# Kernel tuning notes

Measured on AMD Instinct MI355X. Metric: run time of the kernel, lower is better.

Reference implementation:

```python
import jax, jax.numpy as jnp
import numpy as np

EPS = 1e-5
DIM = 128
SCALE = DIM ** (-0.5)


def setup_inputs() -> dict:
    key = jax.random.key(0)
    k1, k2, k3 = jax.random.split(key, 3)
    B, N, D = 2, 128 * 128, DIM
    Q = N // 4
    x = jax.random.normal(k1, (B, N, D), dtype=jnp.float32)
    gamma = jnp.ones((D,), dtype=jnp.float32)
    beta = jnp.zeros((D,), dtype=jnp.float32)
    queries = jax.random.normal(k2, (Q, D), dtype=jnp.float32)
    W = jax.random.normal(k3, (2 * D, D), dtype=jnp.float32) * (1.0 / np.sqrt(D))
    return {"x": x, "gamma": gamma, "beta": beta, "queries": queries, "W": W}


def reference(x, gamma, beta, queries, W):
    # LayerNorm over last dim (eps matches torch default 1e-5)
    mu = jnp.mean(x, axis=-1, keepdims=True)
    var = jnp.mean(jnp.square(x - mu), axis=-1, keepdims=True)
    xn = (x - mu) * jax.lax.rsqrt(var + EPS) * gamma + beta  # [B, N, D]
    # learned-query cross attention: sim = Q @ xn^T * scale -> softmax -> @ xn
    sim = jnp.einsum('qd,bnd->bqn', queries, xn) * SCALE     # [B, Q, N]
    attn = jax.nn.softmax(sim, axis=-1)
    out = jnp.einsum('bqn,bnd->bqd', attn, xn)               # [B, Q, D]
    # trailing linear: dim -> 2*dim, no bias
    return jnp.einsum('bqd,ed->bqe', out, W)                 # [B, Q, 2D]
```

## Files before the change

### kernel.cpp

```cpp
#include <hip/hip_runtime.h>
#include <stdint.h>

#define Nn 16384
#define Dd 128
#define Qq 4096
#define Ee 256
#define NSPLIT 8
#define NCHUNK 2048
#define KV 64
#define NITER 32

typedef __bf16 bf16x8 __attribute__((ext_vector_type(8)));
typedef float floatx16 __attribute__((ext_vector_type(16)));

__device__ __forceinline__ float fexp2(float x) {
#if __has_builtin(__builtin_amdgcn_exp2f)
  return __builtin_amdgcn_exp2f(x);
#else
  return exp2f(x);
#endif
}
__device__ __forceinline__ unsigned pk_bf(float lo, float hi) {
  return __builtin_amdgcn_perm(__float_as_uint(hi) + 0x8000u,
                               __float_as_uint(lo) + 0x8000u, 0x07060302u);
}
__device__ __forceinline__ void stage16(const void* g, void* lds_uniform) {
  __builtin_amdgcn_global_load_lds(
      (const __attribute__((address_space(1))) unsigned int*)g,
      (__attribute__((address_space(3))) unsigned int*)lds_uniform, 16, 0, 0);
}

__global__ __launch_bounds__(256) void k_lnt(
    const float* __restrict__ x, const float* __restrict__ gamma,
    const float* __restrict__ beta, const float* __restrict__ queries,
    const float* __restrict__ W, unsigned* __restrict__ xn,
    unsigned short* __restrict__ xnT, unsigned short* __restrict__ qb,
    unsigned short* __restrict__ wb) {
  __shared__ __align__(16) uint2 lds2[64 * 32];
  const int tid = threadIdx.x;
  const int bid = blockIdx.x;
  const int b = bid >> 8, n0 = (bid & 255) * 64;
  const int r = tid >> 2, qd = tid & 3;

  const float4* xp = (const float4*)(x + ((size_t)(b * Nn + n0 + r)) * Dd + qd * 32);
  float4 v[8];
  float s = 0.f, s2 = 0.f;
#pragma unroll
  for (int i = 0; i < 8; ++i) {
    v[i] = xp[i];
    s += (v[i].x + v[i].y) + (v[i].z + v[i].w);
    s2 += (v[i].x * v[i].x + v[i].y * v[i].y) + (v[i].z * v[i].z + v[i].w * v[i].w);
  }
  s += __shfl_xor(s, 1); s2 += __shfl_xor(s2, 1);
  s += __shfl_xor(s, 2); s2 += __shfl_xor(s2, 2);
  float mu = s * (1.0f / 128.0f);
  float var = s2 * (1.0f / 128.0f) - mu * mu;
  float rs = rsqrtf(var + 1e-5f);

  const float4* gp = (const float4*)(gamma + qd * 32);
  const float4* bp = (const float4*)(beta + qd * 32);
  unsigned pk[16];
#pragma unroll
  for (int i = 0; i < 8; ++i) {
    float4 g = gp[i], bt = bp[i];
    pk[2 * i] = pk_bf((v[i].x - mu) * rs * g.x + bt.x, (v[i].y - mu) * rs * g.y + bt.y);
    pk[2 * i + 1] = pk_bf((v[i].z - mu) * rs * g.z + bt.z, (v[i].w - mu) * rs * g.w + bt.w);
  }
  unsigned* xrow = xn + ((size_t)(b * Nn + n0 + r)) * 64;
#pragma unroll
  for (int j = 0; j < 4; ++j)
    *(uint4*)(xrow + (((qd * 4 + j) ^ (r & 7)) * 4)) =
        make_uint4(pk[4 * j], pk[4 * j + 1], pk[4 * j + 2], pk[4 * j + 3]);
  const int rk = r & 31;
#pragma unroll
  for (int kk = 0; kk < 8; ++kk)
    lds2[r * 32 + ((qd * 8 + kk) ^ rk)] = make_uint2(pk[2 * kk], pk[2 * kk + 1]);
  __syncthreads();
  const int dq = tid >> 3, nc = tid & 7;
  uint2 U[8];
#pragma unroll
  for (int j = 0; j < 8; ++j) {
    int rr = nc * 8 + j;
    U[j] = lds2[rr * 32 + (dq ^ (rr & 31))];
  }
#pragma unroll
  for (int e = 0; e < 4; ++e) {
    int d = dq * 4 + e;
    unsigned a0 = (e & 2) ? U[0].y : U[0].x, a1 = (e & 2) ? U[1].y : U[1].x;
    unsigned a2 = (e & 2) ? U[2].y : U[2].x, a3 = (e & 2) ? U[3].y : U[3].x;
    unsigned a4 = (e & 2) ? U[4].y : U[4].x, a5 = (e & 2) ? U[5].y : U[5].x;
    unsigned a6 = (e & 2) ? U[6].y : U[6].x, a7 = (e & 2) ? U[7].y : U[7].x;
    unsigned sel = (e & 1) ? 0x07060302u : 0x05040100u;
    uint4 o;
    o.x = __builtin_amdgcn_perm(a1, a0, sel);
    o.y = __builtin_amdgcn_perm(a3, a2, sel);
    o.z = __builtin_amdgcn_perm(a5, a4, sel);
    o.w = __builtin_amdgcn_perm(a7, a6, sel);
    *(uint4*)(xnT + ((size_t)(b * Dd + d)) * Nn + n0 + (nc ^ (d & 7)) * 8) = o;
  }
  const float QSC = 0.08838834764831845f * 1.4426950408889634f;
  const int total4 = (Qq * Dd + Ee * Dd) / 4;
  for (int u = bid * 256 + tid; u < total4; u += 512 * 256) {
    if (u < Qq * Dd / 4) {
      float4 v4 = ((const float4*)queries)[u];
      ((uint2*)qb)[u] = make_uint2(pk_bf(v4.x * QSC, v4.y * QSC),
                                   pk_bf(v4.z * QSC, v4.w * QSC));
    } else {
      float4 v4 = ((const float4*)W)[u - Qq * Dd / 4];
      ((uint2*)wb)[u - Qq * Dd / 4] =
          make_uint2(pk_bf(v4.x, v4.y), pk_bf(v4.z, v4.w));
    }
  }
}

__global__ __launch_bounds__(256, 2) void k_attn(
    const unsigned short* __restrict__ xn,
    const unsigned short* __restrict__ xnT,
    const unsigned short* __restrict__ qb,
    float* __restrict__ o_part,
    float* __restrict__ l_part) {
  __shared__ __align__(16) char lds[49152];
  char* lds_x = lds;
  char* lds_xt = lds + 16384;
  char* lds_p = lds + 32768;

  const int bid = blockIdx.x;
  const int split = bid & 7, qt = (bid >> 3) & 31, b = bid >> 8;
  const int tid = threadIdx.x;
  const int wave = tid >> 6, lane = tid & 63;
  const int col = lane & 31, half = lane >> 5;
  const int ck = col & 7;
  const int qwbase = qt * 128 + wave * 32;

  bf16x8 qf[8];
#pragma unroll
  for (int s = 0; s < 8; ++s)
    qf[s] = *(const bf16x8*)(qb + (size_t)(qwbase + col) * Dd + s * 16 + half * 8);

  const floatx16 fz = {0.f,0.f,0.f,0.f,0.f,0.f,0.f,0.f,0.f,0.f,0.f,0.f,0.f,0.f,0.f,0.f};
  floatx16 O[4];
#pragma unroll
  for (int d = 0; d < 4; ++d) O[d] = fz;
  float lsum = 0.f;

  const char* gx = (const char*)xn + (size_t)b * Nn * 256;
  const char* gxt = (const char*)xnT + (size_t)b * Dd * Nn * 2;
  char* ldsp_w = lds_p + wave * 4096;

  for (int i = 0; i < NITER; ++i) {
    const int nb = split * NCHUNK + i * KV;
    const char* xsrc = gx + (size_t)nb * 256;
#pragma unroll
    for (int p = 0; p < 4; ++p) {
      int m = wave * 4 + p;
      stage16(xsrc + m * 1024 + lane * 16, lds_x + m * 1024);
    }
#pragma unroll
    for (int p = 0; p < 4; ++p) {
      int m = wave * 4 + p;
      const char* g = gxt + (size_t)(m * 8 + (lane >> 3)) * (Nn * 2) +
                      (size_t)nb * 2 + (lane & 7) * 16;
      stage16(g, lds_xt + m * 1024);
    }
    __syncthreads();

    floatx16 S[2];
    S[0] = fz; S[1] = fz;
#pragma unroll
    for (int s = 0; s < 8; ++s)
#pragma unroll
      for (int mt = 0; mt < 2; ++mt) {
        bf16x8 ax = *(const bf16x8*)(lds_x + (32 * mt + col) * 256 +
                                     (((2 * s + half) ^ ck) * 16));
        S[mt] = __builtin_amdgcn_mfma_f32_32x32x16_bf16(ax, qf[s], S[mt], 0, 0, 0);
      }

#pragma unroll
    for (int mt = 0; mt < 2; ++mt)
#pragma unroll
      for (int t = 0; t < 4; ++t) {
        float p0 = fexp2(S[mt][4 * t]);
        float p1 = fexp2(S[mt][4 * t + 1]);
        float p2 = fexp2(S[mt][4 * t + 2]);
        float p3 = fexp2(S[mt][4 * t + 3]);
        lsum += (p0 + p1) + (p2 + p3);
        int w = 4 * mt + t;
        *(uint2*)(ldsp_w + col * 128 + ((w ^ ck) * 16) + half * 8) =
            make_uint2(pk_bf(p0, p1), pk_bf(p2, p3));
      }

#pragma unroll
    for (int s2 = 0; s2 < 4; ++s2) {
      bf16x8 ap = *(const bf16x8*)(ldsp_w + col * 128 + (((2 * s2 + half) ^ ck) * 16));
#pragma unroll
      for (int dn = 0; dn < 4; ++dn) {
        bf16x8 bx = *(const bf16x8*)(lds_xt + (32 * dn + col) * 128 +
                                     (((2 * s2 + half) ^ ck) * 16));
        O[dn] = __builtin_amdgcn_mfma_f32_32x32x16_bf16(ap, bx, O[dn], 0, 0, 0);
      }
    }
    __syncthreads();
  }

  float lt = lsum + __shfl_xor(lsum, 32);
  if (half == 0)
    l_part[(size_t)(b * NSPLIT + split) * Qq + qwbase + col] = lt;
  float* op = o_part + ((size_t)(b * NSPLIT + split) * Qq + qwbase) * Dd;
#pragma unroll
  for (int dn = 0; dn < 4; ++dn)
#pragma unroll
    for (int r = 0; r < 16; ++r) {
      int q = (r & 3) + 8 * (r >> 2) + 4 * half;
      op[(size_t)q * Dd + dn * 32 + col] = O[dn][r];
    }
}

__global__ __launch_bounds__(256) void k_comb(
    const float* __restrict__ o_part, const float* __restrict__ l_part,
    const unsigned short* __restrict__ wb, float* __restrict__ out) {
  __shared__ __align__(16) char lds_a[32 * 256];
  __shared__ float lds_linv[32];
  const int bid = blockIdx.x;
  const int b = bid >> 7, qc = bid & 127;
  const int qbase = qc * 32;
  const int tid = threadIdx.x;
  const int wave = tid >> 6, lane = tid & 63;
  const int col = lane & 31, half = lane >> 5;
  const int ck = col & 7;

  if (tid < 32) {
    float l = 0.f;
#pragma unroll
    for (int s = 0; s < 8; ++s)
      l += l_part[(size_t)(b * 8 + s) * Qq + qbase + tid];
    lds_linv[tid] = 1.0f / l;
  }
  __syncthreads();

#pragma unroll
  for (int i = 0; i < 4; ++i) {
    int idx = i * 256 + tid;
    int q = idx >> 5, d4 = idx & 31;
    float4 acc = make_float4(0.f, 0.f, 0.f, 0.f);
#pragma unroll
    for (int s = 0; s < 8; ++s) {
      float4 v = *(const float4*)(o_part + ((size_t)(b * 8 + s) * Qq + qbase + q) * Dd + d4 * 4);
      acc.x += v.x; acc.y += v.y; acc.z += v.z; acc.w += v.w;
    }
    float li = lds_linv[q];
    int w = d4 >> 1;
    int pos = (w & 8) | ((w ^ (q & 7)) & 7);
    *(uint2*)(lds_a + q * 256 + pos * 16 + (d4 & 1) * 8) =
        make_uint2(pk_bf(acc.x * li, acc.y * li), pk_bf(acc.z * li, acc.w * li));
  }
  __syncthreads();

  bf16x8 af[8];
#pragma unroll
  for (int s = 0; s < 8; ++s) {
    int u = 2 * s + half;
    int pos = (u & 8) | ((u ^ ck) & 7);
    af[s] = *(const bf16x8*)(lds_a + col * 256 + pos * 16);
  }

  const floatx16 fz = {0.f,0.f,0.f,0.f,0.f,0.f,0.f,0.f,0.f,0.f,0.f,0.f,0.f,0.f,0.f,0.f};
#pragma unroll
  for (int et = 0; et < 2; ++et) {
    floatx16 C = fz;
    int e_row = wave * 64 + et * 32 + col;
#pragma unroll
    for (int s = 0; s < 8; ++s) {
      bf16x8 bw = *(const bf16x8*)(wb + (size_t)e_row * Dd + s * 16 + half * 8);
      C = __builtin_amdgcn_mfma_f32_32x32x16_bf16(af[s], bw, C, 0, 0, 0);
    }
#pragma unroll
    for (int r = 0; r < 16; ++r) {
      int q = qbase + (r & 3) + 8 * (r >> 2) + 4 * half;
      out[((size_t)b * Qq + q) * Ee + wave * 64 + et * 32 + col] = C[r];
    }
  }
}

extern "C" void kernel_launch(void* const* d_in, const int* in_sizes, int n_in,
                              void* d_out, int out_size, void* d_ws, size_t ws_size,
                              hipStream_t stream) {
  const float* x = (const float*)d_in[0];
  const float* gamma = (const float*)d_in[1];
  const float* beta = (const float*)d_in[2];
  const float* queries = (const float*)d_in[3];
  const float* W = (const float*)d_in[4];
  float* out = (float*)d_out;

  char* w = (char*)d_ws;
  unsigned short* xn = (unsigned short*)(w);
  unsigned short* xnT = (unsigned short*)(w + 8388608);
  unsigned short* qb = (unsigned short*)(w + 16777216);
  unsigned short* wb = (unsigned short*)(w + 17825792);
  float* o_part = (float*)(w + 17891328);
  float* l_part = (float*)(w + 51445760);

  k_lnt<<<dim3(512), dim3(256), 0, stream>>>(x, gamma, beta, queries, W,
                                             (unsigned*)xn, xnT, qb, wb);
  k_attn<<<dim3(512), dim3(256), 0, stream>>>(xn, xnT, qb, o_part, l_part);
  k_comb<<<dim3(256), dim3(256), 0, stream>>>(o_part, l_part, wb, out);
}
```

Before: 168.1 us.

## Pre-tile xn into MFMA fragment order and widen attention query tiles

The layernorm kernel now writes xn and its transpose as contiguous 16KB per-64-row tiles already laid out in MFMA fragment order, so attention staging becomes linear copies with simple LDS addressing. Each attention wave now handles 64 queries instead of 32, reusing every staged K/V tile for twice the MFMA work. The split count can rise to 16 when workspace allows, keeping the grid at 512 blocks. Query and W bf16 conversion moves into the attention and combine kernels, dropping the extra pass in k_lnt. In exchange, register pressure and LDS use (64KB) go up, partial-sum traffic doubles with 16 splits, and W is reconverted by every combine block.

```diff
diff --git a/kernel.cpp b/kernel.cpp
--- a/kernel.cpp
+++ b/kernel.cpp
@@ -5,10 +5,6 @@
 #define Dd 128
 #define Qq 4096
 #define Ee 256
-#define NSPLIT 8
-#define NCHUNK 2048
-#define KV 64
-#define NITER 32
 
 typedef __bf16 bf16x8 __attribute__((ext_vector_type(8)));
 typedef float floatx16 __attribute__((ext_vector_type(16)));
@@ -32,17 +28,15 @@
 
 __global__ __launch_bounds__(256) void k_lnt(
     const float* __restrict__ x, const float* __restrict__ gamma,
-    const float* __restrict__ beta, const float* __restrict__ queries,
-    const float* __restrict__ W, unsigned* __restrict__ xn,
-    unsigned short* __restrict__ xnT, unsigned short* __restrict__ qb,
-    unsigned short* __restrict__ wb) {
+    const float* __restrict__ beta, char* __restrict__ xn_t,
+    char* __restrict__ xnT_t) {
   __shared__ __align__(16) uint2 lds2[64 * 32];
   const int tid = threadIdx.x;
   const int bid = blockIdx.x;
-  const int b = bid >> 8, n0 = (bid & 255) * 64;
+  const int b = bid >> 8, t = bid & 255;
   const int r = tid >> 2, qd = tid & 3;
 
-  const float4* xp = (const float4*)(x + ((size_t)(b * Nn + n0 + r)) * Dd + qd * 32);
+  const float4* xp = (const float4*)(x + ((size_t)(b * Nn + t * 64 + r)) * Dd + qd * 32);
   float4 v[8];
   float s = 0.f, s2 = 0.f;
 #pragma unroll
@@ -59,166 +53,166 @@
 
   const float4* gp = (const float4*)(gamma + qd * 32);
   const float4* bp = (const float4*)(beta + qd * 32);
-  unsigned pk[16];
+  const int rk = r & 31;
 #pragma unroll
   for (int i = 0; i < 8; ++i) {
     float4 g = gp[i], bt = bp[i];
-    pk[2 * i] = pk_bf((v[i].x - mu) * rs * g.x + bt.x, (v[i].y - mu) * rs * g.y + bt.y);
-    pk[2 * i + 1] = pk_bf((v[i].z - mu) * rs * g.z + bt.z, (v[i].w - mu) * rs * g.w + bt.w);
-  }
-  unsigned* xrow = xn + ((size_t)(b * Nn + n0 + r)) * 64;
-#pragma unroll
-  for (int j = 0; j < 4; ++j)
-    *(uint4*)(xrow + (((qd * 4 + j) ^ (r & 7)) * 4)) =
-        make_uint4(pk[4 * j], pk[4 * j + 1], pk[4 * j + 2], pk[4 * j + 3]);
-  const int rk = r & 31;
-#pragma unroll
-  for (int kk = 0; kk < 8; ++kk)
-    lds2[r * 32 + ((qd * 8 + kk) ^ rk)] = make_uint2(pk[2 * kk], pk[2 * kk + 1]);
+    unsigned lo = pk_bf((v[i].x - mu) * rs * g.x + bt.x, (v[i].y - mu) * rs * g.y + bt.y);
+    unsigned hi = pk_bf((v[i].z - mu) * rs * g.z + bt.z, (v[i].w - mu) * rs * g.w + bt.w);
+    lds2[r * 32 + ((qd * 8 + i) ^ rk)] = make_uint2(lo, hi);
+  }
   __syncthreads();
-  const int dq = tid >> 3, nc = tid & 7;
-  uint2 U[8];
-#pragma unroll
-  for (int j = 0; j < 8; ++j) {
-    int rr = nc * 8 + j;
-    U[j] = lds2[rr * 32 + (dq ^ (rr & 31))];
-  }
+
+  const size_t tb = ((size_t)(b * 256 + t)) * 16384;
+#pragma unroll
+  for (int p = 0; p < 4; ++p) {
+    int u = p * 256 + tid;
+    int kv = ((u >> 9) & 1) * 32 + (u & 31);
+    int du = ((u >> 6) & 7) * 2 + ((u >> 5) & 1);
+    uint2 a = lds2[kv * 32 + ((2 * du) ^ (kv & 31))];
+    uint2 c = lds2[kv * 32 + ((2 * du + 1) ^ (kv & 31))];
+    *(uint4*)(xn_t + tb + (size_t)u * 16) = make_uint4(a.x, a.y, c.x, c.y);
+  }
+  const int d = ((tid >> 6) << 5) + (tid & 31);
+  const int klow = (tid >> 5) & 1;
+  const int m0 = d >> 2;
+  const unsigned sel = (d & 1) ? 0x07060302u : 0x05040100u;
 #pragma unroll
   for (int e = 0; e < 4; ++e) {
-    int d = dq * 4 + e;
-    unsigned a0 = (e & 2) ? U[0].y : U[0].x, a1 = (e & 2) ? U[1].y : U[1].x;
-    unsigned a2 = (e & 2) ? U[2].y : U[2].x, a3 = (e & 2) ? U[3].y : U[3].x;
-    unsigned a4 = (e & 2) ? U[4].y : U[4].x, a5 = (e & 2) ? U[5].y : U[5].x;
-    unsigned a6 = (e & 2) ? U[6].y : U[6].x, a7 = (e & 2) ? U[7].y : U[7].x;
-    unsigned sel = (e & 1) ? 0x07060302u : 0x05040100u;
+    int kvu = 2 * e + klow;
+    unsigned wv[8];
+#pragma unroll
+    for (int j = 0; j < 8; ++j) {
+      int kv = kvu * 8 + j;
+      uint2 uu = lds2[kv * 32 + (m0 ^ (kv & 31))];
+      wv[j] = (d & 2) ? uu.y : uu.x;
+    }
     uint4 o;
-    o.x = __builtin_amdgcn_perm(a1, a0, sel);
-    o.y = __builtin_amdgcn_perm(a3, a2, sel);
-    o.z = __builtin_amdgcn_perm(a5, a4, sel);
-    o.w = __builtin_amdgcn_perm(a7, a6, sel);
-    *(uint4*)(xnT + ((size_t)(b * Dd + d)) * Nn + n0 + (nc ^ (d & 7)) * 8) = o;
-  }
-  const float QSC = 0.08838834764831845f * 1.4426950408889634f;
-  const int total4 = (Qq * Dd + Ee * Dd) / 4;
-  for (int u = bid * 256 + tid; u < total4; u += 512 * 256) {
-    if (u < Qq * Dd / 4) {
-      float4 v4 = ((const float4*)queries)[u];
-      ((uint2*)qb)[u] = make_uint2(pk_bf(v4.x * QSC, v4.y * QSC),
-                                   pk_bf(v4.z * QSC, v4.w * QSC));
-    } else {
-      float4 v4 = ((const float4*)W)[u - Qq * Dd / 4];
-      ((uint2*)wb)[u - Qq * Dd / 4] =
-          make_uint2(pk_bf(v4.x, v4.y), pk_bf(v4.z, v4.w));
-    }
+    o.x = __builtin_amdgcn_perm(wv[1], wv[0], sel);
+    o.y = __builtin_amdgcn_perm(wv[3], wv[2], sel);
+    o.z = __builtin_amdgcn_perm(wv[5], wv[4], sel);
+    o.w = __builtin_amdgcn_perm(wv[7], wv[6], sel);
+    *(uint4*)(xnT_t + tb + ((size_t)(tid >> 6)) * 4096 + e * 1024 + klow * 512 +
+              (tid & 31) * 16) = o;
   }
 }
 
 __global__ __launch_bounds__(256, 2) void k_attn(
-    const unsigned short* __restrict__ xn,
-    const unsigned short* __restrict__ xnT,
-    const unsigned short* __restrict__ qb,
+    const char* __restrict__ xn_t, const char* __restrict__ xnT_t,
+    const float* __restrict__ queries,
     float* __restrict__ o_part,
-    float* __restrict__ l_part) {
-  __shared__ __align__(16) char lds[49152];
+    float* __restrict__ l_part,
+    int ns_log2, int niter) {
+  __shared__ __align__(16) char lds[65536];
   char* lds_x = lds;
   char* lds_xt = lds + 16384;
   char* lds_p = lds + 32768;
 
   const int bid = blockIdx.x;
-  const int split = bid & 7, qt = (bid >> 3) & 31, b = bid >> 8;
+  const int ns = 1 << ns_log2;
+  const int split = bid & (ns - 1);
+  const int qt = (bid >> ns_log2) & 15;
+  const int b = bid >> (ns_log2 + 4);
   const int tid = threadIdx.x;
   const int wave = tid >> 6, lane = tid & 63;
   const int col = lane & 31, half = lane >> 5;
-  const int ck = col & 7;
-  const int qwbase = qt * 128 + wave * 32;
-
-  bf16x8 qf[8];
-#pragma unroll
-  for (int s = 0; s < 8; ++s)
-    qf[s] = *(const bf16x8*)(qb + (size_t)(qwbase + col) * Dd + s * 16 + half * 8);
+  const int qwbase = qt * 256 + wave * 64;
+
+  const float QSC = 0.08838834764831845f * 1.4426950408889634f;
+  uint4 qfr[16];
+#pragma unroll
+  for (int g = 0; g < 2; ++g)
+#pragma unroll
+    for (int s = 0; s < 8; ++s) {
+      const float4* qp = (const float4*)(queries +
+          (size_t)(qwbase + g * 32 + col) * Dd + s * 16 + half * 8);
+      float4 q0 = qp[0], q1 = qp[1];
+      qfr[g * 8 + s] = make_uint4(
+          pk_bf(q0.x * QSC, q0.y * QSC), pk_bf(q0.z * QSC, q0.w * QSC),
+          pk_bf(q1.x * QSC, q1.y * QSC), pk_bf(q1.z * QSC, q1.w * QSC));
+    }
 
   const floatx16 fz = {0.f,0.f,0.f,0.f,0.f,0.f,0.f,0.f,0.f,0.f,0.f,0.f,0.f,0.f,0.f,0.f};
-  floatx16 O[4];
-#pragma unroll
-  for (int d = 0; d < 4; ++d) O[d] = fz;
-  float lsum = 0.f;
-
-  const char* gx = (const char*)xn + (size_t)b * Nn * 256;
-  const char* gxt = (const char*)xnT + (size_t)b * Dd * Nn * 2;
-  char* ldsp_w = lds_p + wave * 4096;
-
-  for (int i = 0; i < NITER; ++i) {
-    const int nb = split * NCHUNK + i * KV;
-    const char* xsrc = gx + (size_t)nb * 256;
+  floatx16 O[8];
+#pragma unroll
+  for (int k = 0; k < 8; ++k) O[k] = fz;
+  float ls0 = 0.f, ls1 = 0.f;
+
+  const char* gx = xn_t + ((size_t)(b * 256 + split * niter)) * 16384;
+  const char* gxt = xnT_t + ((size_t)(b * 256 + split * niter)) * 16384;
+  char* pw = lds_p + wave * 8192;
+
+  for (int i = 0; i < niter; ++i) {
+    const size_t ib = (size_t)i * 16384;
 #pragma unroll
     for (int p = 0; p < 4; ++p) {
       int m = wave * 4 + p;
-      stage16(xsrc + m * 1024 + lane * 16, lds_x + m * 1024);
-    }
-#pragma unroll
-    for (int p = 0; p < 4; ++p) {
-      int m = wave * 4 + p;
-      const char* g = gxt + (size_t)(m * 8 + (lane >> 3)) * (Nn * 2) +
-                      (size_t)nb * 2 + (lane & 7) * 16;
-      stage16(g, lds_xt + m * 1024);
+      stage16(gx + ib + m * 1024 + lane * 16, lds_x + m * 1024);
+      stage16(gxt + ib + m * 1024 + lane * 16, lds_xt + m * 1024);
     }
     __syncthreads();
 
-    floatx16 S[2];
-    S[0] = fz; S[1] = fz;
-#pragma unroll
-    for (int s = 0; s < 8; ++s)
-#pragma unroll
-      for (int mt = 0; mt < 2; ++mt) {
-        bf16x8 ax = *(const bf16x8*)(lds_x + (32 * mt + col) * 256 +
-                                     (((2 * s + half) ^ ck) * 16));
-        S[mt] = __builtin_amdgcn_mfma_f32_32x32x16_bf16(ax, qf[s], S[mt], 0, 0, 0);
+#pragma unroll
+    for (int kb = 0; kb < 2; ++kb) {
+      floatx16 S0 = fz, S1 = fz;
+#pragma unroll
+      for (int s = 0; s < 8; ++s) {
+        bf16x8 ax = *(const bf16x8*)(lds_x + kb * 8192 + s * 1024 + half * 512 + col * 16);
+        S0 = __builtin_amdgcn_mfma_f32_32x32x16_bf16(ax, *(const bf16x8*)&qfr[s], S0, 0, 0, 0);
+        S1 = __builtin_amdgcn_mfma_f32_32x32x16_bf16(ax, *(const bf16x8*)&qfr[8 + s], S1, 0, 0, 0);
       }
-
-#pragma unroll
-    for (int mt = 0; mt < 2; ++mt)
-#pragma unroll
-      for (int t = 0; t < 4; ++t) {
-        float p0 = fexp2(S[mt][4 * t]);
-        float p1 = fexp2(S[mt][4 * t + 1]);
-        float p2 = fexp2(S[mt][4 * t + 2]);
-        float p3 = fexp2(S[mt][4 * t + 3]);
-        lsum += (p0 + p1) + (p2 + p3);
-        int w = 4 * mt + t;
-        *(uint2*)(ldsp_w + col * 128 + ((w ^ ck) * 16) + half * 8) =
-            make_uint2(pk_bf(p0, p1), pk_bf(p2, p3));
+#pragma unroll
+      for (int r4 = 0; r4 < 4; ++r4) {
+        float a0 = fexp2(S0[4 * r4 + 0]), a1 = fexp2(S0[4 * r4 + 1]);
+        float a2 = fexp2(S0[4 * r4 + 2]), a3 = fexp2(S0[4 * r4 + 3]);
+        float b0 = fexp2(S1[4 * r4 + 0]), b1 = fexp2(S1[4 * r4 + 1]);
+        float b2 = fexp2(S1[4 * r4 + 2]), b3 = fexp2(S1[4 * r4 + 3]);
+        ls0 += (a0 + a1) + (a2 + a3);
+        ls1 += (b0 + b1) + (b2 + b3);
+        int kvu = 4 * kb + r4;
+        int ofs = (kvu >> 1) * 1024 + (kvu & 1) * 512 + col * 16 + half * 8;
+        *(uint2*)(pw + ofs) = make_uint2(pk_bf(a0, a1), pk_bf(a2, a3));
+        *(uint2*)(pw + 4096 + ofs) = make_uint2(pk_bf(b0, b1), pk_bf(b2, b3));
       }
+    }
 
 #pragma unroll
     for (int s2 = 0; s2 < 4; ++s2) {
-      bf16x8 ap = *(const bf16x8*)(ldsp_w + col * 128 + (((2 * s2 + half) ^ ck) * 16));
+      bf16x8 ap0 = *(const bf16x8*)(pw + s2 * 1024 + half * 512 + col * 16);
+      bf16x8 ap1 = *(const bf16x8*)(pw + 4096 + s2 * 1024 + half * 512 + col * 16);
 #pragma unroll
       for (int dn = 0; dn < 4; ++dn) {
-        bf16x8 bx = *(const bf16x8*)(lds_xt + (32 * dn + col) * 128 +
-                                     (((2 * s2 + half) ^ ck) * 16));
-        O[dn] = __builtin_amdgcn_mfma_f32_32x32x16_bf16(ap, bx, O[dn], 0, 0, 0);
+        bf16x8 bx = *(const bf16x8*)(lds_xt + dn * 4096 + s2 * 1024 + half * 512 + col * 16);
+        O[dn] = __builtin_amdgcn_mfma_f32_32x32x16_bf16(ap0, bx, O[dn], 0, 0, 0);
+        O[4 + dn] = __builtin_amdgcn_mfma_f32_32x32x16_bf16(ap1, bx, O[4 + dn], 0, 0, 0);
       }
     }
     __syncthreads();
   }
 
-  float lt = lsum + __shfl_xor(lsum, 32);
-  if (half == 0)
-    l_part[(size_t)(b * NSPLIT + split) * Qq + qwbase + col] = lt;
-  float* op = o_part + ((size_t)(b * NSPLIT + split) * Qq + qwbase) * Dd;
-#pragma unroll
-  for (int dn = 0; dn < 4; ++dn)
-#pragma unroll
-    for (int r = 0; r < 16; ++r) {
-      int q = (r & 3) + 8 * (r >> 2) + 4 * half;
-      op[(size_t)q * Dd + dn * 32 + col] = O[dn][r];
-    }
+  float lt0 = ls0 + __shfl_xor(ls0, 32);
+  float lt1 = ls1 + __shfl_xor(ls1, 32);
+  if (half == 0) {
+    size_t lb = ((size_t)(b * ns + split)) * Qq + qwbase;
+    l_part[lb + col] = lt0;
+    l_part[lb + 32 + col] = lt1;
+  }
+  float* op = o_part + (((size_t)(b * ns + split)) * Qq + qwbase) * Dd;
+#pragma unroll
+  for (int g = 0; g < 2; ++g)
+#pragma unroll
+    for (int dn = 0; dn < 4; ++dn)
+#pragma unroll
+      for (int r = 0; r < 16; ++r) {
+        int q = g * 32 + (r & 3) + 8 * (r >> 2) + 4 * half;
+        op[(size_t)q * Dd + dn * 32 + col] = O[g * 4 + dn][r];
+      }
 }
 
 __global__ __launch_bounds__(256) void k_comb(
     const float* __restrict__ o_part, const float* __restrict__ l_part,
-    const unsigned short* __restrict__ wb, float* __restrict__ out) {
-  __shared__ __align__(16) char lds_a[32 * 256];
+    const float* __restrict__ W, float* __restrict__ out, int ns) {
+  __shared__ __align__(16) char lds_a[8192];
   __shared__ float lds_linv[32];
   const int bid = blockIdx.x;
   const int b = bid >> 7, qc = bid & 127;
@@ -226,13 +220,23 @@
   const int tid = threadIdx.x;
   const int wave = tid >> 6, lane = tid & 63;
   const int col = lane & 31, half = lane >> 5;
-  const int ck = col & 7;
+
+  uint4 wfr[16];
+#pragma unroll
+  for (int et = 0; et < 2; ++et)
+#pragma unroll
+    for (int s = 0; s < 8; ++s) {
+      const float4* wp = (const float4*)(W +
+          (size_t)(wave * 64 + et * 32 + col) * Dd + s * 16 + half * 8);
+      float4 w0 = wp[0], w1 = wp[1];
+      wfr[et * 8 + s] = make_uint4(pk_bf(w0.x, w0.y), pk_bf(w0.z, w0.w),
+                                   pk_bf(w1.x, w1.y), pk_bf(w1.z, w1.w));
+    }
 
   if (tid < 32) {
     float l = 0.f;
-#pragma unroll
-    for (int s = 0; s < 8; ++s)
-      l += l_part[(size_t)(b * 8 + s) * Qq + qbase + tid];
+    for (int s = 0; s < ns; ++s)
+      l += l_part[(size_t)(b * ns + s) * Qq + qbase + tid];
     lds_linv[tid] = 1.0f / l;
   }
   __syncthreads();
@@ -242,15 +246,15 @@
     int idx = i * 256 + tid;
     int q = idx >> 5, d4 = idx & 31;
     float4 acc = make_float4(0.f, 0.f, 0.f, 0.f);
-#pragma unroll
-    for (int s = 0; s < 8; ++s) {
-      float4 v = *(const float4*)(o_part + ((size_t)(b * 8 + s) * Qq + qbase + q) * Dd + d4 * 4);
+    for (int s = 0; s < ns; ++s) {
+      float4 v = *(const float4*)(o_part +
+          ((size_t)(b * ns + s) * Qq + qbase + q) * Dd + d4 * 4);
       acc.x += v.x; acc.y += v.y; acc.z += v.z; acc.w += v.w;
     }
     float li = lds_linv[q];
-    int w = d4 >> 1;
-    int pos = (w & 8) | ((w ^ (q & 7)) & 7);
-    *(uint2*)(lds_a + q * 256 + pos * 16 + (d4 & 1) * 8) =
+    int du = d4 >> 1;
+    int pos = (du >> 1) * 1024 + (du & 1) * 512 + ((q ^ (du & 7)) & 31) * 16 + (d4 & 1) * 8;
+    *(uint2*)(lds_a + pos) =
         make_uint2(pk_bf(acc.x * li, acc.y * li), pk_bf(acc.z * li, acc.w * li));
   }
   __syncthreads();
@@ -258,19 +262,17 @@
   bf16x8 af[8];
 #pragma unroll
   for (int s = 0; s < 8; ++s) {
-    int u = 2 * s + half;
-    int pos = (u & 8) | ((u ^ ck) & 7);
-    af[s] = *(const bf16x8*)(lds_a + col * 256 + pos * 16);
+    int du = 2 * s + half;
+    af[s] = *(const bf16x8*)(lds_a + s * 1024 + half * 512 + ((col ^ (du & 7)) & 31) * 16);
   }
 
   const floatx16 fz = {0.f,0.f,0.f,0.f,0.f,0.f,0.f,0.f,0.f,0.f,0.f,0.f,0.f,0.f,0.f,0.f};
 #pragma unroll
   for (int et = 0; et < 2; ++et) {
     floatx16 C = fz;
-    int e_row = wave * 64 + et * 32 + col;
 #pragma unroll
     for (int s = 0; s < 8; ++s) {
-      bf16x8 bw = *(const bf16x8*)(wb + (size_t)e_row * Dd + s * 16 + half * 8);
+      bf16x8 bw = *(const bf16x8*)&wfr[et * 8 + s];
       C = __builtin_amdgcn_mfma_f32_32x32x16_bf16(af[s], bw, C, 0, 0, 0);
     }
 #pragma unroll
@@ -292,15 +294,20 @@
   float* out = (float*)d_out;
 
   char* w = (char*)d_ws;
-  unsigned short* xn = (unsigned short*)(w);
-  unsigned short* xnT = (unsigned short*)(w + 8388608);
-  unsigned short* qb = (unsigned short*)(w + 16777216);
-  unsigned short* wb = (unsigned short*)(w + 17825792);
-  float* o_part = (float*)(w + 17891328);
-  float* l_part = (float*)(w + 51445760);
-
-  k_lnt<<<dim3(512), dim3(256), 0, stream>>>(x, gamma, beta, queries, W,
-                                             (unsigned*)xn, xnT, qb, wb);
-  k_attn<<<dim3(512), dim3(256), 0, stream>>>(xn, xnT, qb, o_part, l_part);
-  k_comb<<<dim3(256), dim3(256), 0, stream>>>(o_part, l_part, wb, out);
-}
+  char* xn_t = w;
+  char* xnT_t = w + (size_t)8 * 1024 * 1024;
+  float* o_part = (float*)(w + (size_t)16 * 1024 * 1024);
+
+  const size_t need16 = (size_t)16 * 1024 * 1024 +
+                        (size_t)2 * 16 * Qq * Dd * 4 + (size_t)2 * 16 * Qq * 4;
+  int ns_log2 = (ws_size >= need16) ? 4 : 3;
+  int ns = 1 << ns_log2;
+  int niter = 256 / ns;
+  float* l_part = (float*)(w + (size_t)16 * 1024 * 1024 +
+                           (size_t)2 * ns * Qq * Dd * 4);
+
+  k_lnt<<<dim3(512), dim3(256), 0, stream>>>(x, gamma, beta, xn_t, xnT_t);
+  k_attn<<<dim3(2 * 16 * ns), dim3(256), 0, stream>>>(xn_t, xnT_t, queries,
+                                                      o_part, l_part, ns_log2, niter);
+  k_comb<<<dim3(256), dim3(256), 0, stream>>>(o_part, l_part, W, out, ns);
+}
```

New measurement: 208.4 us. 1.24x slower.
